# Optimization experiments

Measured on AMD Instinct MI355X. Metric: run time of the kernel, lower is better.

## Reference

```python
import jax, jax.numpy as jnp
import numpy as np

H = 1024      # hidden_dim
NH = 16       # num_heads
HD = H // NH  # head_dim
EPS = 1e-12
SCALE = float(np.sqrt(H))


def setup_inputs() -> dict:
    key = jax.random.key(0)
    ks = jax.random.split(key, 12)
    S, B = 2048, 2
    inp = {
        "query": jax.random.normal(ks[0], (S, B, 2 * H), jnp.float32),
        "key":   jax.random.normal(ks[1], (S, B, H), jnp.float32),
        "value": jax.random.normal(ks[2], (S, B, H), jnp.float32),
        # gating params (zeros in torch init, but randomize for a meaningful test)
        "qs": jax.random.normal(ks[3], (1, 1, H), jnp.float32) * 0.02,
        "ks_p": jax.random.normal(ks[4], (1, 1, H), jnp.float32) * 0.02,
        "vs": jax.random.normal(ks[5], (1, 1, H), jnp.float32) * 0.02,
        # Overparam vq: Linear(H, 2H)
        "vq_w": jax.random.normal(ks[6], (2 * H, H), jnp.float32) * (1.0 / np.sqrt(H)),
        "vq_b": jax.random.normal(ks[7], (2 * H,), jnp.float32) * 0.02,
        # q_linear: Linear(2H, H)
        "ql_w": jax.random.normal(ks[8], (H, 2 * H), jnp.float32) * (1.0 / np.sqrt(2 * H)),
        "ql_b": jax.random.normal(ks[9], (H,), jnp.float32) * 0.02,
        # LayerNorm(H)
        "ln_g": jnp.ones((H,), jnp.float32),
        "ln_b": jnp.zeros((H,), jnp.float32),
    }
    return inp


def _layernorm(x, g, b):
    mu = jnp.mean(x, axis=-1, keepdims=True)
    var = jnp.mean(jnp.square(x - mu), axis=-1, keepdims=True)
    return (x - mu) * jax.lax.rsqrt(var + EPS) * g + b


def reference(query, key, value, qs, ks_p, vs, vq_w, vq_b, ql_w, ql_b, ln_g, ln_b):
    # gate vectors
    qsig = jax.nn.sigmoid(qs)            # [1,1,H]
    ksig = jax.nn.sigmoid(ks_p)          # [1,1,H]
    # vq = Overparam(sigmoid(vs)): c,f = l1(x).split(H); sigmoid(f)*tanh(c)
    h = jax.nn.sigmoid(vs) @ vq_w.T + vq_b   # [1,1,2H]
    c, f = h[..., :H], h[..., H:]
    vsig = jax.nn.sigmoid(f) * jnp.tanh(c)   # [1,1,H]

    q = qsig * _layernorm(query @ ql_w.T + ql_b, ln_g, ln_b)  # [S,B,H]
    k = ksig * key
    v = vsig * value

    # batch-first
    q = jnp.transpose(q, (1, 0, 2))  # [B,Q,H]
    k = jnp.transpose(k, (1, 0, 2))  # [B,K,H]
    v = jnp.transpose(v, (1, 0, 2))
    B, Q, _ = q.shape
    K = k.shape[1]

    qh = q.reshape(B, Q, NH, HD)
    kh = k.reshape(B, K, NH, HD)
    vh = v.reshape(B, K, NH, HD)

    scores = jnp.einsum('bqhd,bkhd->bhqk', qh, kh) / SCALE
    w = jax.nn.softmax(scores, axis=-1)                # [B,NH,Q,K]
    out = jnp.einsum('bhqk,bkhd->bqhd', w, vh).reshape(B, Q, H)
    # torch code's final .transpose(0,1) is not assigned -> output is [Q,B,H]
    return jnp.transpose(out, (1, 0, 2))
```

## Files before the change

### kernel.cpp

```cpp
#include <hip/hip_runtime.h>

typedef __bf16 bf16x8 __attribute__((ext_vector_type(8)));
typedef float f32x4 __attribute__((ext_vector_type(4)));
typedef unsigned short u16x8 __attribute__((ext_vector_type(8)));
typedef unsigned short u16x4 __attribute__((ext_vector_type(4)));
typedef unsigned short u16;
typedef unsigned int u32;


#define LOG2E 1.4426950408889634f

__device__ __forceinline__ float b2f(u16 u) {
  union { unsigned int i; float f; } x; x.i = ((unsigned int)u) << 16; return x.f;
}
__device__ __forceinline__ u16 f2b(float f) {
  union { float f; unsigned int i; } x; x.f = f;
  unsigned int r = (x.i + 0x7fffu + ((x.i >> 16) & 1u)) >> 16;
  return (u16)r;
}
__device__ __forceinline__ float sigm(float x) { return 1.0f / (1.0f + __expf(-x)); }
__device__ __forceinline__ u32 cvtpk(float lo, float hi) {
  u32 r; asm("v_cvt_pk_bf16_f32 %0, %1, %2" : "=v"(r) : "v"(lo), "v"(hi)); return r;
}

__device__ __forceinline__ void async16(u16* lds, const u16* g) {
  __builtin_amdgcn_global_load_lds((const __attribute__((address_space(1))) void*)g,
                                   (__attribute__((address_space(3))) void*)lds, 16, 0, 0);
}

__global__ __launch_bounds__(256) void k_cvt_h(const float4* __restrict__ q, u16x4* __restrict__ qd,
                                               const float4* __restrict__ w, u16x4* __restrict__ wd,
                                               const float4* __restrict__ k, u16x4* __restrict__ kd,
                                               const float4* __restrict__ v, u16x4* __restrict__ vd,
                                               const float* __restrict__ vs,
                                               const float* __restrict__ vq_w,
                                               const float* __restrict__ vq_b,
                                               float* __restrict__ h,
                                               const float* __restrict__ qs,
                                               const float* __restrict__ ks,
                                               float* __restrict__ gate) {
  __shared__ float svs[1024];
  int b = blockIdx.x;
  int t = threadIdx.x;
  if (b < 2048) {
#pragma unroll
    for (int vb = b; vb < 18432; vb += 2048) {
      const float4* s; u16x4* d; int i;
      if (vb < 8192)       { s = q; d = qd; i = vb * 256 + t; }
      else if (vb < 10240) { s = w; d = wd; i = (vb - 8192) * 256 + t; }
      else if (vb < 14336) { s = k; d = kd; i = (vb - 10240) * 256 + t; }
      else                 { s = v; d = vd; i = (vb - 14336) * 256 + t; }
      float4 x = s[i];
      u16x4 o; o[0] = f2b(x.x); o[1] = f2b(x.y); o[2] = f2b(x.z); o[3] = f2b(x.w);
      d[i] = o;
    }
    return;
  }
  if (b < 2560) {
    for (int i = t; i < 1024; i += 256) svs[i] = sigm(vs[i]);
    __syncthreads();
    int wave = t >> 6, lane = t & 63;
    int row = (b - 2048) * 4 + wave;
    const float4* w4 = (const float4*)(vq_w + (size_t)row * 1024);
    const float4* s4 = (const float4*)svs;
    float acc = 0.f;
#pragma unroll
    for (int kk = 0; kk < 4; ++kk) {
      float4 wv = w4[kk * 64 + lane];
      float4 sv = s4[kk * 64 + lane];
      acc += wv.x * sv.x + wv.y * sv.y + wv.z * sv.z + wv.w * sv.w;
    }
#pragma unroll
    for (int off = 1; off < 64; off <<= 1) acc += __shfl_xor(acc, off);
    if (lane == 0) h[row] = acc + vq_b[row];
    return;
  }
  int ch = (b - 2560) * 256 + t;
  gate[ch] = sigm(qs[ch]) * sigm(ks[ch]) * (LOG2E / 32.0f);
}

__global__ __launch_bounds__(256) void k_gemm(const u16* __restrict__ A,
                                              const u16* __restrict__ Bt,
                                              u16* __restrict__ C) {
  __shared__ __align__(16) u16 As[64 * 32];
  __shared__ __align__(16) u16 Bs[128 * 32];
  int tid = threadIdx.x;
  int wave = tid >> 6, lane = tid & 63;
  int l15 = lane & 15, quad = lane >> 4;
  int bx = blockIdx.x & 511;
  int kh = blockIdx.x >> 9;
  int kofs = kh << 10;
  int m0 = (bx >> 3) * 64;
  int n0 = (bx & 7) * 128;
  int wm = (wave >> 1) * 32, wn = (wave & 1) * 64;
  f32x4 acc[2][4] = {};
  int c1 = tid, c2 = tid + 256;
  const u16* gaA = A + (size_t)(m0 + (c1 >> 2)) * 2048 + kofs + (c1 & 3) * 8;
  const u16* gb1 = Bt + (size_t)(n0 + (c1 >> 2)) * 2048 + kofs + (c1 & 3) * 8;
  const u16* gb2 = Bt + (size_t)(n0 + (c2 >> 2)) * 2048 + kofs + (c2 & 3) * 8;
  u16* lA1 = As + wave * 512;
  u16* lB1 = Bs + wave * 512;
  u16* lB2 = Bs + 2048 + wave * 512;
  for (int kt = 0; kt < 32; ++kt) {
    async16(lA1, gaA);
    async16(lB1, gb1); async16(lB2, gb2);
    gaA += 32; gb1 += 32; gb2 += 32;
    __syncthreads();
    bf16x8 af[2], bfr[4];
#pragma unroll
    for (int mt = 0; mt < 2; ++mt)
      af[mt] = *(const bf16x8*)(As + (wm + mt * 16 + l15) * 32 + quad * 8);
#pragma unroll
    for (int nt = 0; nt < 4; ++nt)
      bfr[nt] = *(const bf16x8*)(Bs + (wn + nt * 16 + l15) * 32 + quad * 8);
#pragma unroll
    for (int mt = 0; mt < 2; ++mt)
#pragma unroll
      for (int nt = 0; nt < 4; ++nt)
        acc[mt][nt] = __builtin_amdgcn_mfma_f32_16x16x32_bf16(af[mt], bfr[nt], acc[mt][nt], 0, 0, 0);
    __syncthreads();
  }
  u16* Cp = C + (size_t)kh * 4096 * 1024;
#pragma unroll
  for (int mt = 0; mt < 2; ++mt) {
#pragma unroll
    for (int r = 0; r < 4; ++r) {
      int m = m0 + wm + mt * 16 + quad * 4 + r;
      u16* crow = Cp + (size_t)m * 1024 + n0 + wn + l15;
#pragma unroll
      for (int nt = 0; nt < 4; ++nt) crow[nt * 16] = f2b(acc[mt][nt][r]);
    }
  }
}

__global__ __launch_bounds__(256) void k_ln(const u16* __restrict__ qpre0,
                                            const u16* __restrict__ qpre1,
                                            const float* __restrict__ ql_b,
                                            const float* __restrict__ ln_g,
                                            const float* __restrict__ ln_b,
                                            const float* __restrict__ gate,
                                            u16* __restrict__ qatt) {
  int t = threadIdx.x;
  int wave = t >> 6, lane = t & 63;
  int row = blockIdx.x * 4 + wave;
  int ch0 = lane * 16;
  const u16* p0 = qpre0 + (size_t)row * 1024 + ch0;
  const u16* p1 = qpre1 + (size_t)row * 1024 + ch0;
  u16x8 a0 = *(const u16x8*)p0;
  u16x8 a1 = *(const u16x8*)(p0 + 8);
  u16x8 c0 = *(const u16x8*)p1;
  u16x8 c1 = *(const u16x8*)(p1 + 8);
  float qb[16];
#pragma unroll
  for (int i = 0; i < 4; ++i) *(float4*)&qb[i * 4] = *(const float4*)(ql_b + ch0 + i * 4);
  float v[16];
  float s = 0.f, ss = 0.f;
#pragma unroll
  for (int j = 0; j < 8; ++j) {
    v[j] = b2f(a0[j]) + b2f(c0[j]) + qb[j];
    v[8 + j] = b2f(a1[j]) + b2f(c1[j]) + qb[8 + j];
  }
#pragma unroll
  for (int j = 0; j < 16; ++j) { s += v[j]; ss += v[j] * v[j]; }
#pragma unroll
  for (int off = 1; off < 64; off <<= 1) { s += __shfl_xor(s, off); ss += __shfl_xor(ss, off); }
  float mu = s * (1.f / 1024.f);
  float rstd = rsqrtf(ss * (1.f / 1024.f) - mu * mu + 1e-12f);
  float g_[16], bb[16], gt[16];
#pragma unroll
  for (int i = 0; i < 4; ++i) {
    *(float4*)&g_[i * 4] = *(const float4*)(ln_g + ch0 + i * 4);
    *(float4*)&bb[i * 4] = *(const float4*)(ln_b + ch0 + i * 4);
    *(float4*)&gt[i * 4] = *(const float4*)(gate + ch0 + i * 4);
  }
  int sidx = row >> 1, b = row & 1;
  int hh = ch0 >> 6, hd0 = ch0 & 63;
  u16* dst = qatt + ((size_t)(b * 16 + hh) * 2048 + sidx) * 64 + hd0;
  u16x8 o0, o1;
#pragma unroll
  for (int j = 0; j < 8; ++j) {
    o0[j] = f2b(((v[j] - mu) * rstd * g_[j] + bb[j]) * gt[j]);
    o1[j] = f2b(((v[8 + j] - mu) * rstd * g_[8 + j] + bb[8 + j]) * gt[8 + j]);
  }
  *(u16x8*)dst = o0;
  *(u16x8*)(dst + 8) = o1;
}

__device__ __forceinline__ f32x4 mfma16(bf16x8 a, bf16x8 b, f32x4 c) {
  return __builtin_amdgcn_mfma_f32_16x16x32_bf16(a, b, c, 0, 0, 0);
}

template <int CUR>
__device__ __forceinline__ void attn_iter(bool pref,
                                          const bf16x8 (&qf)[2][2],
                                          const u16*& kp, const u16*& vp,
                                          u16 (&Ks)[2][64 * 64], u16 (&Vt)[2][64 * 64],
                                          f32x4 (&oacc)[2][4], float (&l_i)[2],
                                          int kdst, int chbase, int pcol,
                                          int l15, int colA, int colB) {
  f32x4 sacc[2][4] = {};
  const u16* kt0 = Ks[CUR];
  __builtin_amdgcn_s_setprio(1);
#pragma unroll
  for (int nt = 0; nt < 4; ++nt) {
    const u16* krow = kt0 + (nt * 16 + l15) * 64;
    bf16x8 kA = *(const bf16x8*)(krow + colA);
    bf16x8 kB = *(const bf16x8*)(krow + colB);
    sacc[0][nt] = mfma16(kA, qf[0][0], sacc[0][nt]);
    sacc[0][nt] = mfma16(kB, qf[0][1], sacc[0][nt]);
    sacc[1][nt] = mfma16(kA, qf[1][0], sacc[1][nt]);
    sacc[1][nt] = mfma16(kB, qf[1][1], sacc[1][nt]);
  }
  __builtin_amdgcn_s_setprio(0);
  u16x8 kr0, kr1, va, vq;
  if (pref) {
    kp += 64 * 2048;
    kr0 = *(const u16x8*)kp;
    kr1 = *(const u16x8*)(kp + (size_t)32 * 2048);
    vp += 64 * 2048;
    va = *(const u16x8*)vp;
    vq = *(const u16x8*)(vp + 2048);
  }
  u32 pw[2][8];
#pragma unroll
  for (int f = 0; f < 2; ++f) {
    float pe[4][4];
    float ls = 0.f;
#pragma unroll
    for (int nt = 0; nt < 4; ++nt) {
#pragma unroll
      for (int r = 0; r < 4; ++r) pe[nt][r] = __builtin_amdgcn_exp2f(sacc[f][nt][r]);
      ls += (pe[nt][0] + pe[nt][1]) + (pe[nt][2] + pe[nt][3]);
    }
    l_i[f] += ls;
    pw[f][0] = cvtpk(pe[0][0], pe[0][1]); pw[f][1] = cvtpk(pe[0][2], pe[0][3]);
    pw[f][2] = cvtpk(pe[1][0], pe[1][1]); pw[f][3] = cvtpk(pe[1][2], pe[1][3]);
    pw[f][4] = cvtpk(pe[2][0], pe[2][1]); pw[f][5] = cvtpk(pe[2][2], pe[2][3]);
    pw[f][6] = cvtpk(pe[3][0], pe[3][1]); pw[f][7] = cvtpk(pe[3][2], pe[3][3]);
  }
  union U8 { u32 w[4]; bf16x8 v; };
  bf16x8 pa[2][2];
#pragma unroll
  for (int f = 0; f < 2; ++f) {
    U8 t0; t0.w[0] = pw[f][0]; t0.w[1] = pw[f][1]; t0.w[2] = pw[f][2]; t0.w[3] = pw[f][3];
    U8 t1; t1.w[0] = pw[f][4]; t1.w[1] = pw[f][5]; t1.w[2] = pw[f][6]; t1.w[3] = pw[f][7];
    pa[f][0] = t0.v; pa[f][1] = t1.v;
  }
  const u16* vt0 = Vt[CUR];
  __builtin_amdgcn_s_setprio(1);
#pragma unroll
  for (int nt = 0; nt < 4; ++nt) {
    const u16* vrow = vt0 + (nt * 16 + l15) * 64;
    bf16x8 vA = *(const bf16x8*)(vrow + colA);
    bf16x8 vB = *(const bf16x8*)(vrow + colB);
    oacc[0][nt] = mfma16(pa[0][0], vA, oacc[0][nt]);
    oacc[0][nt] = mfma16(pa[0][1], vB, oacc[0][nt]);
    oacc[1][nt] = mfma16(pa[1][0], vA, oacc[1][nt]);
    oacc[1][nt] = mfma16(pa[1][1], vB, oacc[1][nt]);
  }
  __builtin_amdgcn_s_setprio(0);
  if (pref) {
    u16* kd = (u16*)Ks[CUR ^ 1];
    *(u16x8*)(kd + kdst) = kr0;
    *(u16x8*)(kd + kdst + 2048) = kr1;
    u16* vd = (u16*)Vt[CUR ^ 1];
#pragma unroll
    for (int c = 0; c < 8; ++c) {
      u32 pk2 = (u32)va[c] | ((u32)vq[c] << 16);
      *(u32*)&vd[(chbase + c) * 64 + (pcol ^ (c << 3))] = pk2;
    }
  }
  __syncthreads();
}

__global__ __launch_bounds__(256, 2) void k_attn(const u16* __restrict__ qatt,
                                                 const u16* __restrict__ key,
                                                 const u16* __restrict__ value,
                                                 const float* __restrict__ hbuf,
                                                 float* __restrict__ out) {
  int bh = blockIdx.x & 31;
  int qt = blockIdx.x >> 5;
  int b = bh >> 4, h = bh & 15;
  int tid = threadIdx.x, wave = tid >> 6, lane = tid & 63;
  int l15 = lane & 15, quad = lane >> 4;
  int q0 = qt * 128;

  __shared__ __align__(16) u16 Ks[2][64 * 64];
  __shared__ __align__(16) u16 Vt[2][64 * 64];

  bf16x8 qf[2][2];
#pragma unroll
  for (int f = 0; f < 2; ++f) {
    const u16* qrow = qatt + ((size_t)bh * 2048 + q0 + f * 64 + wave * 16 + l15) * 64 + quad * 8;
    qf[f][0] = *(const bf16x8*)qrow;
    qf[f][1] = *(const bf16x8*)(qrow + 32);
  }

  const u16* kb = key + (size_t)b * 1024 + (size_t)h * 64;
  const u16* vb = value + (size_t)b * 1024 + (size_t)h * 64;

  int krow = tid >> 3;
  int kchk = (tid & 7) * 8;
  const u16* kp = kb + (size_t)krow * 2048 + kchk;
  int kdst = krow * 64 + (kchk ^ ((krow & 7) << 3));

  int p = lane & 31;
  int chbase = wave * 16 + (lane >> 5) * 8;
  const u16* vp = vb + (size_t)2 * p * 2048 + chbase;
  int kk = 2 * p;
  int pcol = ((kk >> 5) & 1) * 32 + ((kk >> 2) & 3) * 8 + ((kk >> 4) & 1) * 4 + (kk & 3);
  int swr = (l15 & 7) << 3;
  int colA = (8 * quad) ^ swr;
  int colB = (32 + 8 * quad) ^ swr;

  {
    u16x8 kr0 = *(const u16x8*)kp;
    u16x8 kr1 = *(const u16x8*)(kp + (size_t)32 * 2048);
    *(u16x8*)(&Ks[0][kdst]) = kr0;
    *(u16x8*)(&Ks[0][kdst + 2048]) = kr1;
    u16x8 va = *(const u16x8*)vp;
    u16x8 vq = *(const u16x8*)(vp + 2048);
#pragma unroll
    for (int c = 0; c < 8; ++c) {
      u32 pk2 = (u32)va[c] | ((u32)vq[c] << 16);
      *(u32*)&Vt[0][(chbase + c) * 64 + (pcol ^ (c << 3))] = pk2;
    }
  }
  __syncthreads();

  f32x4 oacc[2][4] = {};
  float l_i[2] = {};

  for (int kt = 0; kt < 32; kt += 2) {
    attn_iter<0>(true, qf, kp, vp, Ks, Vt, oacc, l_i, kdst, chbase, pcol, l15, colA, colB);
    attn_iter<1>(kt < 30, qf, kp, vp, Ks, Vt, oacc, l_i, kdst, chbase, pcol, l15, colA, colB);
  }

#pragma unroll
  for (int f = 0; f < 2; ++f) {
    float l = l_i[f];
    l += __shfl_xor(l, 16);
    l += __shfl_xor(l, 32);
    l_i[f] = l;
  }
  float vsg[4];
#pragma unroll
  for (int nt = 0; nt < 4; ++nt) {
    int ch = h * 64 + nt * 16 + l15;
    vsg[nt] = sigm(hbuf[1024 + ch]) * tanhf(hbuf[ch]);
  }
#pragma unroll
  for (int f = 0; f < 2; ++f)
#pragma unroll
    for (int r = 0; r < 4; ++r) {
      int sq = q0 + f * 64 + wave * 16 + quad * 4 + r;
      float inv = 1.0f / __shfl(l_i[f], quad * 4 + r);
      float* orow = out + ((size_t)sq * 2 + b) * 1024 + h * 64;
#pragma unroll
      for (int nt = 0; nt < 4; ++nt)
        orow[nt * 16 + l15] = oacc[f][nt][r] * inv * vsg[nt];
    }
}

extern "C" void kernel_launch(void* const* d_in, const int* in_sizes, int n_in,
                              void* d_out, int out_size, void* d_ws, size_t ws_size,
                              hipStream_t stream) {
  (void)in_sizes; (void)n_in; (void)out_size; (void)ws_size;
  const float* query = (const float*)d_in[0];
  const float* key   = (const float*)d_in[1];
  const float* value = (const float*)d_in[2];
  const float* qs    = (const float*)d_in[3];
  const float* ksp   = (const float*)d_in[4];
  const float* vs    = (const float*)d_in[5];
  const float* vq_w  = (const float*)d_in[6];
  const float* vq_b  = (const float*)d_in[7];
  const float* ql_w  = (const float*)d_in[8];
  const float* ql_b  = (const float*)d_in[9];
  const float* ln_g  = (const float*)d_in[10];
  const float* ln_b  = (const float*)d_in[11];
  float* out = (float*)d_out;

  float* ws = (float*)d_ws;
  float* h    = ws;
  float* gate = ws + 2048;
  u16* qpre  = (u16*)(ws + 4096);
  u16* qbf   = qpre + (size_t)2 * 4096 * 1024;
  u16* qatt  = qbf;
  u16* wbf   = qbf + (size_t)4096 * 2048;
  u16* kbf   = wbf + (size_t)1024 * 2048;
  u16* vbf   = kbf + (size_t)4096 * 1024;

  hipLaunchKernelGGL(k_cvt_h, dim3(2564), dim3(256), 0, stream,
                     (const float4*)query, (u16x4*)qbf,
                     (const float4*)ql_w,  (u16x4*)wbf,
                     (const float4*)key,   (u16x4*)kbf,
                     (const float4*)value, (u16x4*)vbf,
                     vs, vq_w, vq_b, h, qs, ksp, gate);
  hipLaunchKernelGGL(k_gemm, dim3(1024), dim3(256), 0, stream, qbf, wbf, qpre);
  hipLaunchKernelGGL(k_ln,   dim3(1024), dim3(256), 0, stream, qpre, qpre + (size_t)4096 * 1024,
                     ql_b, ln_g, ln_b, gate, qatt);
  hipLaunchKernelGGL(k_attn, dim3(512),  dim3(256), 0, stream, qatt, kbf, vbf, h, out);
}
```

Baseline: 215.3 us.

## Double-buffer GEMM LDS and split attention waves across key halves

The GEMM now double-buffers its shared-memory tiles so the async load of the next K slice is issued before computing the current one, which removes one barrier per iteration. The attention kernel changes its wave split. Each wave now handles 64 queries against half of each 64-key tile, instead of 16 queries against the full tile, so K and V fragment loads are reused across four query fragments. The partial outputs and row sums are then combined through shared memory at the end. This cuts LDS fragment reads per MFMA but adds a cross-wave reduction and more accumulator registers under a two-blocks-per-SM launch bound.

```diff
diff --git a/kernel.cpp b/kernel.cpp
--- a/kernel.cpp
+++ b/kernel.cpp
@@ -82,8 +82,8 @@
 __global__ __launch_bounds__(256) void k_gemm(const u16* __restrict__ A,
                                               const u16* __restrict__ Bt,
                                               u16* __restrict__ C) {
-  __shared__ __align__(16) u16 As[64 * 32];
-  __shared__ __align__(16) u16 Bs[128 * 32];
+  __shared__ __align__(16) u16 As[2][64 * 32];
+  __shared__ __align__(16) u16 Bs[2][128 * 32];
   int tid = threadIdx.x;
   int wave = tid >> 6, lane = tid & 63;
   int l15 = lane & 15, quad = lane >> 4;
@@ -98,21 +98,25 @@
   const u16* gaA = A + (size_t)(m0 + (c1 >> 2)) * 2048 + kofs + (c1 & 3) * 8;
   const u16* gb1 = Bt + (size_t)(n0 + (c1 >> 2)) * 2048 + kofs + (c1 & 3) * 8;
   const u16* gb2 = Bt + (size_t)(n0 + (c2 >> 2)) * 2048 + kofs + (c2 & 3) * 8;
-  u16* lA1 = As + wave * 512;
-  u16* lB1 = Bs + wave * 512;
-  u16* lB2 = Bs + 2048 + wave * 512;
+  int lofs = wave * 512;
+  async16(As[0] + lofs, gaA);
+  async16(Bs[0] + lofs, gb1); async16(Bs[0] + 2048 + lofs, gb2);
+  gaA += 32; gb1 += 32; gb2 += 32;
+  __syncthreads();
   for (int kt = 0; kt < 32; ++kt) {
-    async16(lA1, gaA);
-    async16(lB1, gb1); async16(lB2, gb2);
-    gaA += 32; gb1 += 32; gb2 += 32;
-    __syncthreads();
+    int cur = kt & 1;
+    if (kt < 31) {
+      async16(As[cur ^ 1] + lofs, gaA);
+      async16(Bs[cur ^ 1] + lofs, gb1); async16(Bs[cur ^ 1] + 2048 + lofs, gb2);
+      gaA += 32; gb1 += 32; gb2 += 32;
+    }
     bf16x8 af[2], bfr[4];
 #pragma unroll
     for (int mt = 0; mt < 2; ++mt)
-      af[mt] = *(const bf16x8*)(As + (wm + mt * 16 + l15) * 32 + quad * 8);
+      af[mt] = *(const bf16x8*)(As[cur] + (wm + mt * 16 + l15) * 32 + quad * 8);
 #pragma unroll
     for (int nt = 0; nt < 4; ++nt)
-      bfr[nt] = *(const bf16x8*)(Bs + (wn + nt * 16 + l15) * 32 + quad * 8);
+      bfr[nt] = *(const bf16x8*)(Bs[cur] + (wn + nt * 16 + l15) * 32 + quad * 8);
 #pragma unroll
     for (int mt = 0; mt < 2; ++mt)
 #pragma unroll
@@ -192,24 +196,25 @@
 
 template <int CUR>
 __device__ __forceinline__ void attn_iter(bool pref,
-                                          const bf16x8 (&qf)[2][2],
+                                          const bf16x8 (&qf)[4][2],
                                           const u16*& kp, const u16*& vp,
                                           u16 (&Ks)[2][64 * 64], u16 (&Vt)[2][64 * 64],
-                                          f32x4 (&oacc)[2][4], float (&l_i)[2],
+                                          f32x4 (&oacc)[4][4], float (&l_i)[4],
                                           int kdst, int chbase, int pcol,
-                                          int l15, int colA, int colB) {
-  f32x4 sacc[2][4] = {};
-  const u16* kt0 = Ks[CUR];
+                                          int l15, int kh, int kcolA, int kcolB, int vcol) {
+  const u16* kt0 = Ks[CUR] + (kh * 32 + l15) * 64;
+  bf16x8 kA0 = *(const bf16x8*)(kt0 + kcolA);
+  bf16x8 kB0 = *(const bf16x8*)(kt0 + kcolB);
+  bf16x8 kA1 = *(const bf16x8*)(kt0 + 16 * 64 + kcolA);
+  bf16x8 kB1 = *(const bf16x8*)(kt0 + 16 * 64 + kcolB);
+  f32x4 sacc[4][2] = {};
   __builtin_amdgcn_s_setprio(1);
 #pragma unroll
-  for (int nt = 0; nt < 4; ++nt) {
-    const u16* krow = kt0 + (nt * 16 + l15) * 64;
-    bf16x8 kA = *(const bf16x8*)(krow + colA);
-    bf16x8 kB = *(const bf16x8*)(krow + colB);
-    sacc[0][nt] = mfma16(kA, qf[0][0], sacc[0][nt]);
-    sacc[0][nt] = mfma16(kB, qf[0][1], sacc[0][nt]);
-    sacc[1][nt] = mfma16(kA, qf[1][0], sacc[1][nt]);
-    sacc[1][nt] = mfma16(kB, qf[1][1], sacc[1][nt]);
+  for (int f = 0; f < 4; ++f) {
+    sacc[f][0] = mfma16(kA0, qf[f][0], sacc[f][0]);
+    sacc[f][0] = mfma16(kB0, qf[f][1], sacc[f][0]);
+    sacc[f][1] = mfma16(kA1, qf[f][0], sacc[f][1]);
+    sacc[f][1] = mfma16(kB1, qf[f][1], sacc[f][1]);
   }
   __builtin_amdgcn_s_setprio(0);
   u16x8 kr0, kr1, va, vq;
@@ -221,42 +226,31 @@
     va = *(const u16x8*)vp;
     vq = *(const u16x8*)(vp + 2048);
   }
-  u32 pw[2][8];
-#pragma unroll
-  for (int f = 0; f < 2; ++f) {
-    float pe[4][4];
-    float ls = 0.f;
-#pragma unroll
-    for (int nt = 0; nt < 4; ++nt) {
-#pragma unroll
-      for (int r = 0; r < 4; ++r) pe[nt][r] = __builtin_amdgcn_exp2f(sacc[f][nt][r]);
-      ls += (pe[nt][0] + pe[nt][1]) + (pe[nt][2] + pe[nt][3]);
-    }
-    l_i[f] += ls;
-    pw[f][0] = cvtpk(pe[0][0], pe[0][1]); pw[f][1] = cvtpk(pe[0][2], pe[0][3]);
-    pw[f][2] = cvtpk(pe[1][0], pe[1][1]); pw[f][3] = cvtpk(pe[1][2], pe[1][3]);
-    pw[f][4] = cvtpk(pe[2][0], pe[2][1]); pw[f][5] = cvtpk(pe[2][2], pe[2][3]);
-    pw[f][6] = cvtpk(pe[3][0], pe[3][1]); pw[f][7] = cvtpk(pe[3][2], pe[3][3]);
-  }
   union U8 { u32 w[4]; bf16x8 v; };
-  bf16x8 pa[2][2];
-#pragma unroll
-  for (int f = 0; f < 2; ++f) {
-    U8 t0; t0.w[0] = pw[f][0]; t0.w[1] = pw[f][1]; t0.w[2] = pw[f][2]; t0.w[3] = pw[f][3];
-    U8 t1; t1.w[0] = pw[f][4]; t1.w[1] = pw[f][5]; t1.w[2] = pw[f][6]; t1.w[3] = pw[f][7];
-    pa[f][0] = t0.v; pa[f][1] = t1.v;
+  bf16x8 pa[4];
+#pragma unroll
+  for (int f = 0; f < 4; ++f) {
+    float pe[2][4];
+#pragma unroll
+    for (int kn = 0; kn < 2; ++kn)
+#pragma unroll
+      for (int r = 0; r < 4; ++r) pe[kn][r] = __builtin_amdgcn_exp2f(sacc[f][kn][r]);
+    l_i[f] += (pe[0][0] + pe[0][1] + pe[0][2] + pe[0][3]) +
+              (pe[1][0] + pe[1][1] + pe[1][2] + pe[1][3]);
+    U8 t;
+    t.w[0] = cvtpk(pe[0][0], pe[0][1]); t.w[1] = cvtpk(pe[0][2], pe[0][3]);
+    t.w[2] = cvtpk(pe[1][0], pe[1][1]); t.w[3] = cvtpk(pe[1][2], pe[1][3]);
+    pa[f] = t.v;
   }
   const u16* vt0 = Vt[CUR];
   __builtin_amdgcn_s_setprio(1);
 #pragma unroll
   for (int nt = 0; nt < 4; ++nt) {
-    const u16* vrow = vt0 + (nt * 16 + l15) * 64;
-    bf16x8 vA = *(const bf16x8*)(vrow + colA);
-    bf16x8 vB = *(const bf16x8*)(vrow + colB);
-    oacc[0][nt] = mfma16(pa[0][0], vA, oacc[0][nt]);
-    oacc[0][nt] = mfma16(pa[0][1], vB, oacc[0][nt]);
-    oacc[1][nt] = mfma16(pa[1][0], vA, oacc[1][nt]);
-    oacc[1][nt] = mfma16(pa[1][1], vB, oacc[1][nt]);
+    bf16x8 vF = *(const bf16x8*)(vt0 + (nt * 16 + l15) * 64 + vcol);
+    oacc[0][nt] = mfma16(pa[0], vF, oacc[0][nt]);
+    oacc[1][nt] = mfma16(pa[1], vF, oacc[1][nt]);
+    oacc[2][nt] = mfma16(pa[2], vF, oacc[2][nt]);
+    oacc[3][nt] = mfma16(pa[3], vF, oacc[3][nt]);
   }
   __builtin_amdgcn_s_setprio(0);
   if (pref) {
@@ -283,15 +277,17 @@
   int b = bh >> 4, h = bh & 15;
   int tid = threadIdx.x, wave = tid >> 6, lane = tid & 63;
   int l15 = lane & 15, quad = lane >> 4;
+  int qh = wave >> 1, kh = wave & 1;
   int q0 = qt * 128;
 
   __shared__ __align__(16) u16 Ks[2][64 * 64];
   __shared__ __align__(16) u16 Vt[2][64 * 64];
-
-  bf16x8 qf[2][2];
-#pragma unroll
-  for (int f = 0; f < 2; ++f) {
-    const u16* qrow = qatt + ((size_t)bh * 2048 + q0 + f * 64 + wave * 16 + l15) * 64 + quad * 8;
+  __shared__ float Lx[2][2][32];
+
+  bf16x8 qf[4][2];
+#pragma unroll
+  for (int f = 0; f < 4; ++f) {
+    const u16* qrow = qatt + ((size_t)bh * 2048 + q0 + qh * 64 + f * 16 + l15) * 64 + quad * 8;
     qf[f][0] = *(const bf16x8*)qrow;
     qf[f][1] = *(const bf16x8*)(qrow + 32);
   }
@@ -310,8 +306,9 @@
   int kk = 2 * p;
   int pcol = ((kk >> 5) & 1) * 32 + ((kk >> 2) & 3) * 8 + ((kk >> 4) & 1) * 4 + (kk & 3);
   int swr = (l15 & 7) << 3;
-  int colA = (8 * quad) ^ swr;
-  int colB = (32 + 8 * quad) ^ swr;
+  int kcolA = (8 * quad) ^ swr;
+  int kcolB = (32 + 8 * quad) ^ swr;
+  int vcol = (kh * 32 + 8 * quad) ^ swr;
 
   {
     u16x8 kr0 = *(const u16x8*)kp;
@@ -328,38 +325,57 @@
   }
   __syncthreads();
 
-  f32x4 oacc[2][4] = {};
-  float l_i[2] = {};
+  f32x4 oacc[4][4] = {};
+  float l_i[4] = {};
 
   for (int kt = 0; kt < 32; kt += 2) {
-    attn_iter<0>(true, qf, kp, vp, Ks, Vt, oacc, l_i, kdst, chbase, pcol, l15, colA, colB);
-    attn_iter<1>(kt < 30, qf, kp, vp, Ks, Vt, oacc, l_i, kdst, chbase, pcol, l15, colA, colB);
-  }
-
-#pragma unroll
-  for (int f = 0; f < 2; ++f) {
+    attn_iter<0>(true, qf, kp, vp, Ks, Vt, oacc, l_i, kdst, chbase, pcol, l15, kh, kcolA, kcolB, vcol);
+    attn_iter<1>(kt < 30, qf, kp, vp, Ks, Vt, oacc, l_i, kdst, chbase, pcol, l15, kh, kcolA, kcolB, vcol);
+  }
+
+#pragma unroll
+  for (int f = 0; f < 4; ++f) {
     float l = l_i[f];
     l += __shfl_xor(l, 16);
     l += __shfl_xor(l, 32);
     l_i[f] = l;
   }
+  int d = kh ^ 1;
+  float* base = (qh == 0) ? (float*)&Ks[0][0] : (float*)&Vt[0][0];
+  float* Rw = base + d * 2048;
+#pragma unroll
+  for (int ff = 0; ff < 2; ++ff) {
+    int fo = d * 2 + ff;
+#pragma unroll
+    for (int nt = 0; nt < 4; ++nt)
+#pragma unroll
+      for (int r = 0; r < 4; ++r)
+        Rw[(ff * 16 + quad * 4 + r) * 64 + nt * 16 + l15] = oacc[fo][nt][r];
+    if (quad == 0) Lx[qh][d][ff * 16 + l15] = l_i[fo];
+  }
+  __syncthreads();
   float vsg[4];
 #pragma unroll
   for (int nt = 0; nt < 4; ++nt) {
     int ch = h * 64 + nt * 16 + l15;
     vsg[nt] = sigm(hbuf[1024 + ch]) * tanhf(hbuf[ch]);
   }
-#pragma unroll
-  for (int f = 0; f < 2; ++f)
+  float* Rr = base + kh * 2048;
+#pragma unroll
+  for (int ff = 0; ff < 2; ++ff) {
+    int fo = kh * 2 + ff;
+    float lt = l_i[fo] + Lx[qh][kh][ff * 16 + l15];
 #pragma unroll
     for (int r = 0; r < 4; ++r) {
-      int sq = q0 + f * 64 + wave * 16 + quad * 4 + r;
-      float inv = 1.0f / __shfl(l_i[f], quad * 4 + r);
+      int sq = q0 + qh * 64 + kh * 32 + ff * 16 + quad * 4 + r;
+      float inv = 1.0f / __shfl(lt, quad * 4 + r);
       float* orow = out + ((size_t)sq * 2 + b) * 1024 + h * 64;
 #pragma unroll
       for (int nt = 0; nt < 4; ++nt)
-        orow[nt * 16 + l15] = oacc[f][nt][r] * inv * vsg[nt];
-    }
+        orow[nt * 16 + l15] =
+            (oacc[fo][nt][r] + Rr[(ff * 16 + quad * 4 + r) * 64 + nt * 16 + l15]) * inv * vsg[nt];
+    }
+  }
 }
 
 extern "C" void kernel_launch(void* const* d_in, const int* in_sizes, int n_in,
```

Result: slower. 457.0 us (+112.2%).
